# Kernel optimization log

Hardware: AMD Instinct MI355X
Metric: run time of the kernel (lower is better)

Reference implementation:

```python
import jax, jax.numpy as jnp
import numpy as np

N_NODES = 50000

def gcn_conv(x, src, dst, W, b, n_nodes):
    # PyG GCNConv: add self-loops, symmetric deg^{-1/2} normalization,
    # linear transform, scatter-add aggregation (source -> target), bias.
    loop = jnp.arange(n_nodes, dtype=src.dtype)
    src2 = jnp.concatenate([src, loop])
    dst2 = jnp.concatenate([dst, loop])
    deg = jax.ops.segment_sum(jnp.ones_like(dst2, dtype=x.dtype), dst2, num_segments=n_nodes)
    dinv = jnp.where(deg > 0, jax.lax.rsqrt(deg), 0.0)
    norm = dinv[src2] * dinv[dst2]  # [E + N]
    h = x @ W                        # [N, out]
    msg = h[src2] * norm[:, None]    # gather + scale
    out = jax.ops.segment_sum(msg, dst2, num_segments=n_nodes)
    return out + b

def setup_inputs() -> dict:
    key = jax.random.key(0)
    k1, k2, k3, k4 = jax.random.split(key, 4)
    x = jax.random.normal(k1, (N_NODES, 64), dtype=jnp.float32)
    edge_index = jax.random.randint(k2, (2, 800000), 0, N_NODES, dtype=jnp.int64)
    # Glorot-ish init for weights
    W1 = jax.random.normal(k3, (64, 128), dtype=jnp.float32) * (1.0 / np.sqrt(64))
    b1 = jnp.zeros((128,), dtype=jnp.float32)
    W2 = jax.random.normal(k4, (128, 8), dtype=jnp.float32) * (1.0 / np.sqrt(128))
    b2 = jnp.zeros((8,), dtype=jnp.float32)
    return {"x": x, "edge_index": edge_index, "W1": W1, "b1": b1, "W2": W2, "b2": b2}

def reference(x, edge_index, W1, b1, W2, b2):
    src, dst = edge_index[0], edge_index[1]
    h = gcn_conv(x, src, dst, W1, b1, N_NODES)
    h = jax.nn.relu(h)
    out = gcn_conv(h, src, dst, W2, b2, N_NODES)
    return out
```

## Files before the change

kernel.cpp:

```cpp
#include <hip/hip_runtime.h>

#define IN1 64
#define MID 128
#define OUT2 8
#define YPAD 136
#define CAP 64

__device__ __forceinline__ unsigned short f2bf(float f) {
    unsigned int u = __float_as_uint(f);
    unsigned int r = (u + 0x7fff + ((u >> 16) & 1)) >> 16;
    return (unsigned short)r;
}
__device__ __forceinline__ float bflo(unsigned int u) { return __uint_as_float(u << 16); }
__device__ __forceinline__ float bfhi(unsigned int u) { return __uint_as_float(u & 0xffff0000u); }

__global__ void k_fillp(const int* __restrict__ src, const int* __restrict__ dst,
                        int* __restrict__ cnt, unsigned short* __restrict__ col,
                        int E4, int E) {
    int gid = blockIdx.x * blockDim.x + threadIdx.x;
    if (gid < E4) {
        int4 sv = ((const int4*)src)[gid];
        int4 dv = ((const int4*)dst)[gid];
        int p0 = atomicAdd(&cnt[dv.x], 1); if (p0 < CAP) col[dv.x * CAP + p0] = (unsigned short)sv.x;
        int p1 = atomicAdd(&cnt[dv.y], 1); if (p1 < CAP) col[dv.y * CAP + p1] = (unsigned short)sv.y;
        int p2 = atomicAdd(&cnt[dv.z], 1); if (p2 < CAP) col[dv.z * CAP + p2] = (unsigned short)sv.z;
        int p3 = atomicAdd(&cnt[dv.w], 1); if (p3 < CAP) col[dv.w * CAP + p3] = (unsigned short)sv.w;
    }
    if (gid == 0) {
        for (int e = E4 * 4; e < E; ++e) {
            int d = dst[e];
            int p = atomicAdd(&cnt[d], 1);
            if (p < CAP) col[d * CAP + p] = (unsigned short)src[e];
        }
    }
}

__global__ void k_prescale(const float4* __restrict__ x4, const int* __restrict__ cnt,
                           float* __restrict__ dinv, ushort4* __restrict__ xb4, int n16) {
    int gid = blockIdx.x * blockDim.x + threadIdx.x;
    if (gid >= n16) return;
    int row = gid >> 4;
    float d = rsqrtf((float)(cnt[row] + 1));
    if ((gid & 15) == 0) dinv[row] = d;
    float4 vx = x4[gid];
    ushort4 p;
    p.x = f2bf(vx.x * d); p.y = f2bf(vx.y * d);
    p.z = f2bf(vx.z * d); p.w = f2bf(vx.w * d);
    xb4[gid] = p;
}

__global__ __launch_bounds__(256) void k_node(const uint2* __restrict__ xb2,
                                              const int* __restrict__ cnt,
                                              const unsigned short* __restrict__ col,
                                              const float* __restrict__ dinv,
                                              const float* __restrict__ W1,
                                              const float* __restrict__ b1,
                                              const float* __restrict__ W2,
                                              float* __restrict__ z, int n) {
    __shared__ float w2s[MID * OUT2];
    __shared__ float tS[4][4][IN1];
    __shared__ float yS[4][4][YPAD];

    int t = threadIdx.x;
    ((float4*)w2s)[t] = ((const float4*)W2)[t];

    int lane = t & 63, wave = t >> 6;
    int g = lane >> 4;
    int fl2 = lane & 15;
    int q4 = fl2 & 3;
    int row0 = blockIdx.x * 16 + wave * 4;
    int row = row0 + g;
    bool valid = row < n;

    float a0 = 0.f, a1 = 0.f, a2 = 0.f, a3 = 0.f;
    int deg = 0, base = 0;
    if (valid) {
        deg = min(cnt[row], CAP);
        base = row * CAP;
        uint2 u = xb2[(size_t)row * 16 + fl2];
        a0 = bflo(u.x); a1 = bfhi(u.x); a2 = bflo(u.y); a3 = bfhi(u.y);
    }
    int j = 0;
    for (; j + 4 <= deg; j += 4) {
        int cv = col[base + j + q4];
#pragma unroll
        for (int p = 0; p < 4; ++p) {
            int s = __shfl(cv, (g << 4) + p, 64);
            uint2 u = xb2[(size_t)s * 16 + fl2];
            a0 += bflo(u.x); a1 += bfhi(u.x);
            a2 += bflo(u.y); a3 += bfhi(u.y);
        }
    }
    int rem = deg - j;
    if (rem > 0) {
        int cv = col[base + min(j + q4, CAP - 1)];
#pragma unroll
        for (int p = 0; p < 4; ++p) {
            int s = __shfl(cv, (g << 4) + p, 64);
            if (p < rem) {
                uint2 u = xb2[(size_t)s * 16 + fl2];
                a0 += bflo(u.x); a1 += bfhi(u.x);
                a2 += bflo(u.y); a3 += bfhi(u.y);
            }
        }
    }
    {
        float4 w = {a0, a1, a2, a3};
        *(float4*)&tS[wave][g][4 * fl2] = w;
    }

    float dnd[4];
#pragma unroll
    for (int k = 0; k < 4; ++k) dnd[k] = dinv[min(row0 + k, n - 1)];

    float ya0 = 0.f, yb0 = 0.f, ya1 = 0.f, yb1 = 0.f;
    float ya2 = 0.f, yb2 = 0.f, ya3 = 0.f, yb3 = 0.f;
#pragma unroll 4
    for (int k4 = 0; k4 < IN1; k4 += 4) {
        float4 t0 = *(const float4*)&tS[wave][0][k4];
        float4 t1 = *(const float4*)&tS[wave][1][k4];
        float4 t2 = *(const float4*)&tS[wave][2][k4];
        float4 t3 = *(const float4*)&tS[wave][3][k4];
#pragma unroll
        for (int kk = 0; kk < 4; ++kk) {
            int k = k4 + kk;
            float wa = W1[k * MID + lane];
            float wb = W1[k * MID + lane + 64];
            float e0 = (&t0.x)[kk], e1 = (&t1.x)[kk], e2 = (&t2.x)[kk], e3 = (&t3.x)[kk];
            ya0 = fmaf(e0, wa, ya0); yb0 = fmaf(e0, wb, yb0);
            ya1 = fmaf(e1, wa, ya1); yb1 = fmaf(e1, wb, yb1);
            ya2 = fmaf(e2, wa, ya2); yb2 = fmaf(e2, wb, yb2);
            ya3 = fmaf(e3, wa, ya3); yb3 = fmaf(e3, wb, yb3);
        }
    }
    float bl = b1[lane], bh = b1[lane + 64];
    yS[wave][0][lane] = fmaxf(fmaf(ya0, dnd[0], bl), 0.f);
    yS[wave][0][lane + 64] = fmaxf(fmaf(yb0, dnd[0], bh), 0.f);
    yS[wave][1][lane] = fmaxf(fmaf(ya1, dnd[1], bl), 0.f);
    yS[wave][1][lane + 64] = fmaxf(fmaf(yb1, dnd[1], bh), 0.f);
    yS[wave][2][lane] = fmaxf(fmaf(ya2, dnd[2], bl), 0.f);
    yS[wave][2][lane + 64] = fmaxf(fmaf(yb2, dnd[2], bh), 0.f);
    yS[wave][3][lane] = fmaxf(fmaf(ya3, dnd[3], bl), 0.f);
    yS[wave][3][lane + 64] = fmaxf(fmaf(yb3, dnd[3], bh), 0.f);

    __syncthreads();

    int nd2 = lane >> 4, ch = lane & 15;
    float p[OUT2];
#pragma unroll
    for (int c = 0; c < OUT2; ++c) p[c] = 0.0f;
#pragma unroll
    for (int kk = 0; kk < 8; ++kk) {
        int k = kk * 16 + ch;
        float yk = yS[wave][nd2][k];
        float4 wlo = *(const float4*)&w2s[k * OUT2];
        float4 whi = *(const float4*)&w2s[k * OUT2 + 4];
        p[0] = fmaf(yk, wlo.x, p[0]); p[1] = fmaf(yk, wlo.y, p[1]);
        p[2] = fmaf(yk, wlo.z, p[2]); p[3] = fmaf(yk, wlo.w, p[3]);
        p[4] = fmaf(yk, whi.x, p[4]); p[5] = fmaf(yk, whi.y, p[5]);
        p[6] = fmaf(yk, whi.z, p[6]); p[7] = fmaf(yk, whi.w, p[7]);
    }
#pragma unroll
    for (int off = 1; off < 16; off <<= 1) {
#pragma unroll
        for (int c = 0; c < OUT2; ++c) p[c] += __shfl_xor(p[c], off, 64);
    }
    int rw = row0 + nd2;
    if (rw < n && ch < OUT2) {
        z[(size_t)rw * OUT2 + ch] = p[ch] * dinv[rw];
    }
}

__global__ __launch_bounds__(256) void k_gather2(const int* __restrict__ cnt,
                                                 const unsigned short* __restrict__ col,
                                                 const float* __restrict__ z,
                                                 const float* __restrict__ dinv,
                                                 const float* __restrict__ b2,
                                                 float* __restrict__ out, int n) {
    int t = threadIdx.x, lane = t & 63, wave = t >> 6;
    int node = blockIdx.x * 4 + wave;
    if (node >= n) return;
    int nb = lane >> 3, c = lane & 7;
    float acc = (nb == 0) ? z[(size_t)node * OUT2 + c] : 0.0f;
    int deg = min(cnt[node], CAP);
    int base = node * CAP;
    int j = nb;
    for (; j + 8 < deg; j += 16) {
        int s0 = col[base + j], s1 = col[base + j + 8];
        float a0 = z[(size_t)s0 * OUT2 + c];
        float a1 = z[(size_t)s1 * OUT2 + c];
        acc += a0 + a1;
    }
    if (j < deg) acc += z[(size_t)col[base + j] * OUT2 + c];
#pragma unroll
    for (int off = 8; off < 64; off <<= 1) acc += __shfl_xor(acc, off, 64);
    if (lane < OUT2) out[(size_t)node * OUT2 + lane] = fmaf(acc, dinv[node], b2[lane]);
}

extern "C" void kernel_launch(void* const* d_in, const int* in_sizes, int n_in,
                              void* d_out, int out_size, void* d_ws, size_t ws_size,
                              hipStream_t stream) {
    const float* x  = (const float*)d_in[0];
    const int*   ei = (const int*)d_in[1];
    const float* W1 = (const float*)d_in[2];
    const float* b1 = (const float*)d_in[3];
    const float* W2 = (const float*)d_in[4];
    const float* b2 = (const float*)d_in[5];
    float* out = (float*)d_out;

    int N = in_sizes[0] / IN1;
    int E = in_sizes[1] / 2;
    const int* src = ei;
    const int* dst = ei + E;

    int* cnt = (int*)d_ws;
    unsigned short* col = (unsigned short*)(cnt + N);
    float* dinv = (float*)(col + (size_t)N * CAP);
    float* z = dinv + N;
    unsigned short* xb = (unsigned short*)(z + (size_t)N * OUT2);

    const int B = 256;
    int E4 = E / 4;

    hipMemsetAsync(cnt, 0, (size_t)N * sizeof(int), stream);
    k_fillp<<<(E4 + B - 1) / B, B, 0, stream>>>(src, dst, cnt, col, E4, E);
    k_prescale<<<((size_t)N * 16 + B - 1) / B, B, 0, stream>>>((const float4*)x, cnt, dinv,
                                                               (ushort4*)xb, N * 16);
    k_node<<<(N + 15) / 16, 256, 0, stream>>>((const uint2*)xb, cnt, col, dinv, W1, b1, W2, z, N);
    k_gather2<<<(N + 3) / 4, 256, 0, stream>>>(cnt, col, z, dinv, b2, out, N);
}
```

Before: 171.7 us.

## Partition CSR fill by destination range per XCD to localize atomics

The edge-bucketing kernel now launches 8 groups of 192 slice-blocks, where each group (chosen as blockIdx & 7, intended to map onto one XCD) handles only the destination nodes in its own eighth of the node range. Every block scans its slice of all edges and does atomics and column writes only for destinations it owns, so the atomics on cnt and the col writes for a node range should stay within one XCD's L2. In exchange, the edge arrays are read eight times over and each thread evaluates range predicates on every edge.

```diff
diff --git a/kernel.cpp b/kernel.cpp
--- a/kernel.cpp
+++ b/kernel.cpp
@@ -14,19 +14,37 @@
 __device__ __forceinline__ float bflo(unsigned int u) { return __uint_as_float(u << 16); }
 __device__ __forceinline__ float bfhi(unsigned int u) { return __uint_as_float(u & 0xffff0000u); }
 
-__global__ void k_fillp(const int* __restrict__ src, const int* __restrict__ dst,
-                        int* __restrict__ cnt, unsigned short* __restrict__ col,
-                        int E4, int E) {
-    int gid = blockIdx.x * blockDim.x + threadIdx.x;
-    if (gid < E4) {
-        int4 sv = ((const int4*)src)[gid];
-        int4 dv = ((const int4*)dst)[gid];
-        int p0 = atomicAdd(&cnt[dv.x], 1); if (p0 < CAP) col[dv.x * CAP + p0] = (unsigned short)sv.x;
-        int p1 = atomicAdd(&cnt[dv.y], 1); if (p1 < CAP) col[dv.y * CAP + p1] = (unsigned short)sv.y;
-        int p2 = atomicAdd(&cnt[dv.z], 1); if (p2 < CAP) col[dv.z * CAP + p2] = (unsigned short)sv.z;
-        int p3 = atomicAdd(&cnt[dv.w], 1); if (p3 < CAP) col[dv.w * CAP + p3] = (unsigned short)sv.w;
-    }
-    if (gid == 0) {
+__global__ __launch_bounds__(256) void k_fillp(const int* __restrict__ src,
+                                               const int* __restrict__ dst,
+                                               int* __restrict__ cnt,
+                                               unsigned short* __restrict__ col,
+                                               int E4, int E, int npx, int slices) {
+    int xcd = blockIdx.x & 7;
+    int slice = blockIdx.x >> 3;
+    int lo = xcd * npx, hi = lo + npx;
+    int eps = (E4 + slices - 1) / slices;
+    int g0 = slice * eps, g1 = min(E4, g0 + eps);
+    for (int g = g0 + (int)threadIdx.x; g < g1; g += 256) {
+        int4 sv = ((const int4*)src)[g];
+        int4 dv = ((const int4*)dst)[g];
+        if (dv.x >= lo && dv.x < hi) {
+            int p = atomicAdd(&cnt[dv.x], 1);
+            if (p < CAP) col[dv.x * CAP + p] = (unsigned short)sv.x;
+        }
+        if (dv.y >= lo && dv.y < hi) {
+            int p = atomicAdd(&cnt[dv.y], 1);
+            if (p < CAP) col[dv.y * CAP + p] = (unsigned short)sv.y;
+        }
+        if (dv.z >= lo && dv.z < hi) {
+            int p = atomicAdd(&cnt[dv.z], 1);
+            if (p < CAP) col[dv.z * CAP + p] = (unsigned short)sv.z;
+        }
+        if (dv.w >= lo && dv.w < hi) {
+            int p = atomicAdd(&cnt[dv.w], 1);
+            if (p < CAP) col[dv.w * CAP + p] = (unsigned short)sv.w;
+        }
+    }
+    if (blockIdx.x == 0 && threadIdx.x == 0) {
         for (int e = E4 * 4; e < E; ++e) {
             int d = dst[e];
             int p = atomicAdd(&cnt[d], 1);
@@ -221,9 +239,11 @@
 
     const int B = 256;
     int E4 = E / 4;
+    int npx = (N + 7) / 8;
+    int slices = 192;
 
     hipMemsetAsync(cnt, 0, (size_t)N * sizeof(int), stream);
-    k_fillp<<<(E4 + B - 1) / B, B, 0, stream>>>(src, dst, cnt, col, E4, E);
+    k_fillp<<<slices * 8, B, 0, stream>>>(src, dst, cnt, col, E4, E, npx, slices);
     k_prescale<<<((size_t)N * 16 + B - 1) / B, B, 0, stream>>>((const float4*)x, cnt, dinv,
                                                                (ushort4*)xb, N * 16);
     k_node<<<(N + 15) / 16, 256, 0, stream>>>((const uint2*)xb, cnt, col, dinv, W1, b1, W2, z, N);
```

Result: no change. 169.4 us (-1.4%).
